# Kernel tuning notes

Hardware: AMD Instinct MI355X
Metric: run time of the kernel (lower is better)

## Reference

```python
import jax, jax.numpy as jnp
import numpy as np

D = 128      # memory_dim
L = 64       # segment_len
SCALE = 1.0 / np.sqrt(D)
LN_EPS = 1e-5


def _layernorm(x, g, b):
    mu = x.mean(-1, keepdims=True)
    var = ((x - mu) ** 2).mean(-1, keepdims=True)
    return (x - mu) * jax.lax.rsqrt(var + LN_EPS) * g + b


def setup_inputs() -> dict:
    key = jax.random.key(0)
    ks = jax.random.split(key, 8)
    B, T, Hd = 4, 4096, 2048
    w = 0.02  # init scale for weight matrices
    return {
        "H": jax.random.normal(ks[0], (B, T, Hd), jnp.float32),
        "M": jax.random.normal(ks[1], (B, D, D), jnp.float32),  # [B,K=128,D=128]
        "ln_g": jnp.ones((Hd,), jnp.float32),
        "ln_b": jnp.zeros((Hd,), jnp.float32),
        "W_eta_w": jax.random.normal(ks[2], (Hd,), jnp.float32) * w,
        "W_eta_b": jnp.full((1,), -5.0, jnp.float32),
        "sum_q": jax.random.normal(ks[3], (D,), jnp.float32),
        "sp_w": jax.random.normal(ks[4], (Hd, D), jnp.float32) * w,
        "sp_b": jnp.zeros((D,), jnp.float32),
        "eta_ch": jnp.ones((D,), jnp.float32),
        "temp": jnp.ones((1,), jnp.float32),
        "W_qkv": jax.random.normal(ks[5], (Hd, 3 * D), jnp.float32) * w,
    }


def reference(H, M, ln_g, ln_b, W_eta_w, W_eta_b, sum_q, sp_w, sp_b, eta_ch, temp, W_qkv):
    B, T, _ = H.shape
    K = M.shape[1]
    S = T // L  # T chosen divisible by segment_len (no-pad branch)

    Hn = _layernorm(H, ln_g, ln_b)                      # [B,T,Hd]

    # ---- write_memory ----
    H_mem = Hn @ sp_w + sp_b                            # [B,T,D]
    eta_tokens = jnp.einsum('bth,h->bt', Hn, W_eta_w) + W_eta_b  # [B,T]

    H_segs = H_mem.reshape(B, S, L, D)
    summary_scores = jnp.einsum('d,bsld->bsl', sum_q, H_segs) * SCALE
    summary_w = jax.nn.softmax(summary_scores, axis=-1)
    Z_seg = jnp.einsum('bsl,bsld->bsd', summary_w, H_segs)       # [B,S,D]

    eta_sig = jax.nn.sigmoid(eta_tokens)                          # [B,T]
    eta_seg = eta_sig.reshape(B, S, L).max(axis=-1)[..., None]    # [B,S,1]

    scores = jnp.einsum('bsd,bkd->bsk', Z_seg, M) * SCALE * jnp.exp(temp)
    A = jax.nn.softmax(scores, axis=-1)                           # [B,S,K]
    DeltaM = jnp.einsum('bsk,bsd->bkd', A, Z_seg * eta_seg)       # [B,K,D]

    eta_avg = eta_seg.mean(axis=1, keepdims=True)                 # [B,1,1]
    gate = eta_avg * jax.nn.sigmoid(eta_ch)                       # [B,1,D]
    M_new = (1.0 - gate) * M + DeltaM / S

    norm_sq = jnp.sum(DeltaM ** 2) / S
    # diversity loss on M_new
    Mn = M_new / jnp.maximum(jnp.linalg.norm(M_new, axis=-1, keepdims=True), 1e-12)
    sim = jnp.einsum('bkd,bjd->bkj', Mn, Mn) * (1.0 - jnp.eye(K, dtype=M.dtype))
    div_loss = jnp.mean(sim ** 2)
    loss = norm_sq * 0.01 + div_loss * 0.1

    # ---- read_memory (from updated memory; K<=1024 -> dense softmax path) ----
    Q_r = Hn @ W_qkv[:, 2 * D:]                                   # [B,T,D]
    r_scores = jnp.einsum('btd,bkd->btk', Q_r, M_new)
    A_r = jax.nn.softmax(r_scores * 2.0, axis=-1)
    C = jnp.einsum('btk,bkd->btd', A_r, M_new)                    # [B,T,D]

    return C, loss
```

## Files before the change

### kernel.cpp

```cpp
#include <hip/hip_runtime.h>
#include <hip/hip_bf16.h>
#include <math.h>

#define HD   2048
#define DD   128
#define TT   4096
#define BB   4
#define MT   (BB*TT)
#define LSEG 64
#define SSEG 64
#define NCOL 256
#define SCALE_D 0.088388347648318447f

typedef _Float16 half8 __attribute__((ext_vector_type(8)));
typedef _Float16 half4v __attribute__((ext_vector_type(4)));
typedef float    f32x4 __attribute__((ext_vector_type(4)));

__device__ __forceinline__ float sigmf(float x){ return 1.f/(1.f+__expf(-x)); }

__device__ __forceinline__ void glds16(const void* g, void* l) {
  __builtin_amdgcn_global_load_lds(
      (const __attribute__((address_space(1))) unsigned int*)g,
      (__attribute__((address_space(3))) unsigned int*)l, 16, 0, 0);
}

__global__ void k_pre(const float* __restrict__ ln_g, const float* __restrict__ ln_b,
                      const float* __restrict__ sp_w, const float* __restrict__ sp_b,
                      const float* __restrict__ W_qkv, const float* __restrict__ W_eta_w,
                      const float* __restrict__ W_eta_b,
                      _Float16* __restrict__ Bp, float* __restrict__ s_vec,
                      float* __restrict__ cb_vec, float* __restrict__ we2,
                      float* __restrict__ scal)
{
  __shared__ float red1[256], red2[256];
  int n = blockIdx.x, t = threadIdx.x;
  float sp = 0.f, cp = 0.f;
  if (n < NCOL) {
    for (int h = t; h < HD; h += 256) {
      float w = (n < DD) ? sp_w[(size_t)h*DD + n] : W_qkv[(size_t)h*384 + 256 + (n-DD)];
      float g = ln_g[h], b = ln_b[h];
      Bp[(size_t)n*HD + h] = (_Float16)(g*w);
      sp += g*w; cp += b*w;
    }
  } else {
    for (int h = t; h < HD; h += 256) {
      float w = W_eta_w[h];
      float g = ln_g[h], b = ln_b[h];
      we2[h] = g*w;
      sp += g*w; cp += b*w;
    }
  }
  red1[t] = sp; red2[t] = cp;
  __syncthreads();
  for (int o = 128; o > 0; o >>= 1) {
    if (t < o) { red1[t] += red1[t+o]; red2[t] += red2[t+o]; }
    __syncthreads();
  }
  if (t == 0) {
    if (n < NCOL) {
      s_vec[n]  = red1[0];
      cb_vec[n] = red2[0] + ((n < DD) ? sp_b[n] : 0.f);
    } else {
      scal[0] = red1[0];
      scal[1] = red2[0] + W_eta_b[0];
      scal[2] = 0.f; scal[3] = 0.f;
    }
  }
}

__launch_bounds__(512, 2)
__global__ void k01(const float* __restrict__ H, const _Float16* __restrict__ Bp,
                    const float* __restrict__ s_vec, const float* __restrict__ cb_vec,
                    const float* __restrict__ we2, const float* __restrict__ scal,
                    const float* __restrict__ sum_q, const float* __restrict__ Mmat,
                    const float* __restrict__ temp,
                    float* __restrict__ Q_r, float* __restrict__ Zeta,
                    float* __restrict__ A_seg, float* __restrict__ eta_seg)
{
  __shared__ __align__(16) char pool[81920];
  __shared__ float we_s[HD];
  __shared__ float smu[64], srs[64], seta[64];
  __shared__ float sq_s[128], w64_s[64], Zs[128], red_s[4];
  __shared__ float eta_sh_s;
  _Float16* sA  = (_Float16*)pool;
  _Float16* sB  = (_Float16*)(pool + 16384);
  float*    sHm = (float*)pool;

  int tid = threadIdx.x;
  int seg = blockIdx.x;
  int b   = seg >> 6;
  int m0  = seg * 64;
  int w = tid >> 6, lane = tid & 63;
  int wr = w >> 2, wc = w & 3;
  int fcol = lane & 15, kq = lane >> 4;

  for (int i = tid; i < HD/4; i += 512)
    ((float4*)we_s)[i] = ((const float4*)we2)[i];
  if (tid < 128) sq_s[tid] = sum_q[tid];
  float scal0 = scal[0], scal1 = scal[1];
  __syncthreads();

  int r_l = tid >> 3, s8 = tid & 7;
  const float* aptr = H + (size_t)(m0 + r_l)*HD + s8*8;
  int bn[4], bsl[4];
#pragma unroll
  for (int i = 0; i < 4; ++i) {
    int idx = i*512 + tid;
    bn[i]  = idx >> 3;
    bsl[i] = (idx & 7) ^ (bn[i] & 7);
  }

  f32x4 acc[2][4];
#pragma unroll
  for (int i = 0; i < 2; ++i)
#pragma unroll
    for (int j = 0; j < 4; ++j) acc[i][j] = (f32x4){0.f,0.f,0.f,0.f};
  float s1 = 0.f, s2 = 0.f, se = 0.f;

  float4 pa0 = *(const float4*)(aptr + 0);
  float4 pa1 = *(const float4*)(aptr + 4);
#pragma unroll
  for (int i = 0; i < 4; ++i)
    glds16(Bp + (size_t)bn[i]*HD + bsl[i]*8, sB + (size_t)(i*512 + tid)*8);

  for (int kt = 0; kt < 32; ++kt) {
    int cur = kt & 1;
    int k0 = kt*64;
    _Float16* sAc = sA + cur*4096;
    _Float16* sBc = sB + cur*16384;
    {
      float v[8] = {pa0.x,pa0.y,pa0.z,pa0.w, pa1.x,pa1.y,pa1.z,pa1.w};
      const float4* wv4 = (const float4*)(we_s + k0 + s8*8);
      float4 u0 = wv4[0], u1 = wv4[1];
      float uu[8] = {u0.x,u0.y,u0.z,u0.w, u1.x,u1.y,u1.z,u1.w};
      half8 h0;
#pragma unroll
      for (int j = 0; j < 8; ++j) {
        s1 += v[j]; s2 += v[j]*v[j]; se += v[j]*uu[j];
        h0[j] = (_Float16)v[j];
      }
      *(half8*)&sAc[r_l*64 + (s8 ^ (r_l & 7))*8] = h0;
    }
    if (kt < 31) {
      const float* ap = aptr + (kt+1)*64;
      pa0 = *(const float4*)(ap + 0);
      pa1 = *(const float4*)(ap + 4);
      asm volatile("s_waitcnt vmcnt(2) lgkmcnt(0)" ::: "memory");
    } else {
      asm volatile("s_waitcnt vmcnt(0) lgkmcnt(0)" ::: "memory");
    }
    __builtin_amdgcn_s_barrier();
    __builtin_amdgcn_sched_barrier(0);
    if (kt < 31) {
      _Float16* sBn = sB + (cur^1)*16384;
      const _Float16* bsrc = Bp + (k0 + 64);
#pragma unroll
      for (int i = 0; i < 4; ++i)
        glds16(bsrc + (size_t)bn[i]*HD + bsl[i]*8, sBn + (size_t)(i*512 + tid)*8);
    }
#pragma unroll
    for (int ks = 0; ks < 2; ++ks) {
      half8 af[2], bf[4];
#pragma unroll
      for (int rt = 0; rt < 2; ++rt) {
        int r = wr*32 + rt*16 + fcol;
        int ch = (ks*4 + kq) ^ (r & 7);
        af[rt] = *(half8*)&sAc[r*64 + ch*8];
      }
#pragma unroll
      for (int ct = 0; ct < 4; ++ct) {
        int n = wc*64 + ct*16 + fcol;
        int ch = (ks*4 + kq) ^ (n & 7);
        bf[ct] = *(half8*)&sBc[n*64 + ch*8];
      }
#pragma unroll
      for (int rt = 0; rt < 2; ++rt)
#pragma unroll
        for (int ct = 0; ct < 4; ++ct)
          acc[rt][ct] = __builtin_amdgcn_mfma_f32_16x16x32_f16(af[rt], bf[ct], acc[rt][ct], 0,0,0);
    }
  }

  s1 += __shfl_xor(s1, 1); s1 += __shfl_xor(s1, 2); s1 += __shfl_xor(s1, 4);
  s2 += __shfl_xor(s2, 1); s2 += __shfl_xor(s2, 2); s2 += __shfl_xor(s2, 4);
  se += __shfl_xor(se, 1); se += __shfl_xor(se, 2); se += __shfl_xor(se, 4);
  if (s8 == 0) {
    float mu   = s1 * (1.f/HD);
    float var  = s2 * (1.f/HD) - mu*mu;
    float rstd = rsqrtf(var + 1e-5f);
    smu[r_l] = mu; srs[r_l] = rstd;
    seta[r_l] = rstd*(se - mu*scal0) + scal1;
  }
  __syncthreads();

#pragma unroll
  for (int ct = 0; ct < 4; ++ct) {
    int nl = wc*64 + ct*16 + fcol;
    float sn = s_vec[nl], cbn = cb_vec[nl];
#pragma unroll
    for (int rt = 0; rt < 2; ++rt)
#pragma unroll
      for (int r = 0; r < 4; ++r) {
        int m = wr*32 + rt*16 + kq*4 + r;
        sHm[m*260 + nl] = srs[m]*(acc[rt][ct][r] - smu[m]*sn) + cbn;
      }
  }
  __syncthreads();

#pragma unroll
  for (int j = 0; j < 4; ++j) {
    int idx = j*512 + tid;
    int row = idx >> 5, c4 = (idx & 31)*4;
    *(float4*)&Q_r[(size_t)(m0 + row)*DD + c4] = *(float4*)&sHm[row*260 + 128 + c4];
  }

  if (w == 0) {
    float sc = 0.f;
    const float4* hrow = (const float4*)&sHm[lane*260];
#pragma unroll
    for (int d4 = 0; d4 < 32; ++d4) {
      float4 hv = hrow[d4];
      float4 qv = *(const float4*)&sq_s[d4*4];
      sc += hv.x*qv.x + hv.y*qv.y + hv.z*qv.z + hv.w*qv.w;
    }
    sc *= SCALE_D;
    float mx = sc;
    for (int o = 32; o > 0; o >>= 1) mx = fmaxf(mx, __shfl_xor(mx, o));
    float e = __expf(sc - mx);
    float sm = e;
    for (int o = 32; o > 0; o >>= 1) sm += __shfl_xor(sm, o);
    w64_s[lane] = e / sm;
  } else if (w == 1) {
    float ev = seta[lane];
    for (int o = 32; o > 0; o >>= 1) ev = fmaxf(ev, __shfl_xor(ev, o));
    if (lane == 0) { float es = sigmf(ev); eta_sh_s = es; eta_seg[seg] = es; }
  }
  __syncthreads();

  if (tid < 128) {
    float z = 0.f;
    for (int l = 0; l < 64; ++l) z += w64_s[l]*sHm[l*260 + tid];
    Zs[tid] = z;
    Zeta[(size_t)seg*DD + tid] = z * eta_sh_s;
  }
  __syncthreads();

  float sc2 = 0.f;
  if (tid < 128) {
    const float4* mrow = (const float4*)(Mmat + ((size_t)b*DD + tid)*DD);
#pragma unroll
    for (int d4 = 0; d4 < 32; ++d4) {
      float4 mv = mrow[d4];
      sc2 += mv.x*Zs[d4*4] + mv.y*Zs[d4*4+1] + mv.z*Zs[d4*4+2] + mv.w*Zs[d4*4+3];
    }
    sc2 *= SCALE_D * __expf(temp[0]);
    float mx = sc2;
    for (int o = 32; o > 0; o >>= 1) mx = fmaxf(mx, __shfl_xor(mx, o));
    if (lane == 0) red_s[w] = mx;
  }
  __syncthreads();
  float ev2 = 0.f;
  if (tid < 128) {
    float mx = fmaxf(red_s[0], red_s[1]);
    ev2 = __expf(sc2 - mx);
    float sm = ev2;
    for (int o = 32; o > 0; o >>= 1) sm += __shfl_xor(sm, o);
    if (lane == 0) red_s[2 + w] = sm;
  }
  __syncthreads();
  if (tid < 128) {
    float smt = red_s[2] + red_s[3];
    A_seg[(size_t)seg*DD + tid] = ev2 / smt;
  }
}

__global__ void k2b(const float* __restrict__ A_seg, const float* __restrict__ Zeta,
                    const float* __restrict__ eta_seg, const float* __restrict__ Mmat,
                    const float* __restrict__ eta_ch,
                    float* __restrict__ M_new, float* __restrict__ rns_arr,
                    float* __restrict__ scal)
{
  __shared__ float As[64][33];
  __shared__ __align__(16) float Zsl[64*128];
  __shared__ float rowp[32][8];
  __shared__ float eta_av;
  __shared__ float redb[4];
  int tid = threadIdx.x;
  int b = blockIdx.x >> 2, kq = blockIdx.x & 3;
  for (int i = tid; i < 64*32; i += 256) {
    int s = i >> 5, j = i & 31;
    As[s][j] = A_seg[((size_t)b*SSEG + s)*DD + kq*32 + j];
  }
  const float4* z4 = (const float4*)(Zeta + (size_t)b*SSEG*DD);
  float4* zs4 = (float4*)Zsl;
  for (int i = tid; i < 64*32; i += 256) zs4[i] = z4[i];
  if (tid < 64) {
    float ev = eta_seg[(size_t)b*SSEG + tid];
    for (int o=32;o>0;o>>=1) ev += __shfl_xor(ev, o);
    if (tid == 0) eta_av = ev * (1.f/SSEG);
  }
  __syncthreads();
  int kl = tid & 31, dg = tid >> 5;
  int k = kq*32 + kl, d0 = dg*16;
  float dm[16];
#pragma unroll
  for (int j=0;j<16;j++) dm[j]=0.f;
  for (int s = 0; s < 64; ++s) {
    float a = As[s][kl];
    const float* zr = &Zsl[s*128 + d0];
#pragma unroll
    for (int j=0;j<16;j++) dm[j] += a * zr[j];
  }
  float nsq = 0.f;
#pragma unroll
  for (int j=0;j<16;j++) nsq += dm[j]*dm[j];
  float eav = eta_av;
  float mn[16];
  float ss = 0.f;
#pragma unroll
  for (int j=0;j<16;j++) {
    int d = d0 + j;
    float gate = eav * sigmf(eta_ch[d]);
    float v = (1.f - gate)*Mmat[((size_t)b*DD + k)*DD + d] + dm[j]*(1.f/SSEG);
    mn[j] = v; ss += v*v;
  }
#pragma unroll
  for (int j=0;j<16;j+=4) {
    float4 v4; v4.x=mn[j]; v4.y=mn[j+1]; v4.z=mn[j+2]; v4.w=mn[j+3];
    *(float4*)&M_new[((size_t)b*DD + k)*DD + d0 + j] = v4;
  }
  rowp[kl][dg] = ss;
  for (int o=1;o<64;o<<=1) nsq += __shfl_xor(nsq, o);
  if ((tid&63)==0) redb[tid>>6] = nsq;
  __syncthreads();
  if (tid == 0) atomicAdd(&scal[2], redb[0]+redb[1]+redb[2]+redb[3]);
  if (tid < 32) {
    float t2 = 0.f;
#pragma unroll
    for (int g=0; g<8; ++g) t2 += rowp[tid][g];
    float nrm = sqrtf(t2);
    rns_arr[(size_t)b*DD + kq*32 + tid] = 1.f / fmaxf(nrm, 1e-12f);
  }
}

__global__ void k2d(const float* __restrict__ M_new, const float* __restrict__ rns_arr,
                    float* __restrict__ scal)
{
  __shared__ float kr[4][128];
  __shared__ float redb[4];
  int tid = threadIdx.x;
  int b = blockIdx.x >> 5, kq = blockIdx.x & 31;
  for (int i = tid; i < 4*128; i += 256) {
    int ki = i >> 7, d = i & 127;
    kr[ki][d] = M_new[((size_t)b*DD + kq*4 + ki)*DD + d];
  }
  __syncthreads();
  int j = tid & 127, kh = tid >> 7;
  const float* mj = &M_new[((size_t)b*DD + j)*DD];
  float rj = rns_arr[(size_t)b*DD + j];
  float dv = 0.f;
#pragma unroll
  for (int ki2 = 0; ki2 < 2; ++ki2) {
    int kil = kh*2 + ki2;
    int kk = kq*4 + kil;
    float dot = 0.f;
    for (int d = 0; d < 128; d += 4) {
      float4 a = *(const float4*)(mj + d);
      dot += a.x*kr[kil][d] + a.y*kr[kil][d+1] + a.z*kr[kil][d+2] + a.w*kr[kil][d+3];
    }
    if (kk != j) {
      float sv = dot * rj * rns_arr[(size_t)b*DD + kk];
      dv += sv*sv;
    }
  }
  for (int o=1;o<64;o<<=1) dv += __shfl_xor(dv, o);
  if ((tid&63)==0) redb[tid>>6] = dv;
  __syncthreads();
  if (tid==0) atomicAdd(&scal[3], redb[0]+redb[1]+redb[2]+redb[3]);
}

__launch_bounds__(256, 1)
__global__ void k3(const float* __restrict__ Q_r, const float* __restrict__ M_new,
                   const float* __restrict__ scal, float* __restrict__ out)
{
  __shared__ __align__(16) _Float16 Mq[128*132];
  __shared__ __align__(16) _Float16 Mt[128*136];
  __shared__ __align__(16) _Float16 Ps[64*132];
  int tid = threadIdx.x;
  int b = blockIdx.x >> 6, tile = blockIdx.x & 63;
  int t0 = tile*64;
  if (blockIdx.x == 0 && tid == 0) {
    float loss = 0.01f*(scal[2]*(1.f/SSEG)) + 0.1f*(scal[3]*(1.f/(BB*DD*DD)));
    out[(size_t)MT*DD] = loss;
  }
  const float4* m4 = (const float4*)(M_new + (size_t)b*DD*DD);
#pragma unroll
  for (int it = 0; it < 4; ++it) {
    int sb = it*256 + tid;
    int rb = sb & 31, cb = sb >> 5;
    int r0 = rb*4, c0 = cb*4;
    float a[4][4];
#pragma unroll
    for (int j = 0; j < 4; ++j) {
      float4 v = m4[(size_t)(r0+j)*32 + cb];
      a[j][0]=v.x; a[j][1]=v.y; a[j][2]=v.z; a[j][3]=v.w;
    }
#pragma unroll
    for (int j = 0; j < 4; ++j) {
      half4v h; h.x=(_Float16)a[j][0]; h.y=(_Float16)a[j][1];
                h.z=(_Float16)a[j][2]; h.w=(_Float16)a[j][3];
      *(half4v*)&Mq[(r0+j)*132 + c0] = h;
    }
#pragma unroll
    for (int j2 = 0; j2 < 4; ++j2) {
      half4v h; h.x=(_Float16)a[0][j2]; h.y=(_Float16)a[1][j2];
                h.z=(_Float16)a[2][j2]; h.w=(_Float16)a[3][j2];
      *(half4v*)&Mt[(c0+j2)*136 + r0] = h;
    }
  }
  int w = tid >> 6, lane = tid & 63;
  int fcol = lane & 15, kq = lane >> 4;
  int tokA = t0 + w*16 + fcol;
  size_t qbase = ((size_t)b*TT + tokA)*DD;
  half8 af[4];
#pragma unroll
  for (int ks = 0; ks < 4; ++ks) {
    float4 q0 = *(const float4*)&Q_r[qbase + ks*32 + kq*8];
    float4 q1 = *(const float4*)&Q_r[qbase + ks*32 + kq*8 + 4];
    half8 h;
    h[0]=(_Float16)q0.x; h[1]=(_Float16)q0.y; h[2]=(_Float16)q0.z; h[3]=(_Float16)q0.w;
    h[4]=(_Float16)q1.x; h[5]=(_Float16)q1.y; h[6]=(_Float16)q1.z; h[7]=(_Float16)q1.w;
    af[ks] = h;
  }
  __syncthreads();
  f32x4 sacc[8];
#pragma unroll
  for (int nt = 0; nt < 8; ++nt) sacc[nt] = (f32x4){0.f,0.f,0.f,0.f};
#pragma unroll
  for (int nt = 0; nt < 8; ++nt)
#pragma unroll
    for (int ks = 0; ks < 4; ++ks) {
      half8 bf = *(half8*)&Mq[(nt*16 + fcol)*132 + ks*32 + kq*8];
      sacc[nt] = __builtin_amdgcn_mfma_f32_16x16x32_f16(af[ks], bf, sacc[nt], 0,0,0);
    }
#pragma unroll
  for (int nt = 0; nt < 8; ++nt)
#pragma unroll
    for (int r = 0; r < 4; ++r) sacc[nt][r] *= 2.f;
  float mx[4], sm[4];
#pragma unroll
  for (int r = 0; r < 4; ++r) {
    float m = sacc[0][r];
#pragma unroll
    for (int nt = 1; nt < 8; ++nt) m = fmaxf(m, sacc[nt][r]);
#pragma unroll
    for (int o = 1; o < 16; o <<= 1) m = fmaxf(m, __shfl_xor(m, o));
    mx[r] = m;
  }
#pragma unroll
  for (int r = 0; r < 4; ++r) sm[r] = 0.f;
#pragma unroll
  for (int nt = 0; nt < 8; ++nt)
#pragma unroll
    for (int r = 0; r < 4; ++r) {
      float e = __expf(sacc[nt][r] - mx[r]);
      sacc[nt][r] = e; sm[r] += e;
    }
#pragma unroll
  for (int r = 0; r < 4; ++r) {
    float s = sm[r];
#pragma unroll
    for (int o = 1; o < 16; o <<= 1) s += __shfl_xor(s, o);
    sm[r] = 1.f / s;
  }
#pragma unroll
  for (int nt = 0; nt < 8; ++nt)
#pragma unroll
    for (int r = 0; r < 4; ++r) {
      int tk = w*16 + kq*4 + r;
      Ps[tk*132 + nt*16 + fcol] = (_Float16)(sacc[nt][r]*sm[r]);
    }
  __syncthreads();
  half8 pf[4];
#pragma unroll
  for (int ks = 0; ks < 4; ++ks)
    pf[ks] = *(half8*)&Ps[(w*16 + fcol)*132 + ks*32 + kq*8];
  f32x4 cacc[8];
#pragma unroll
  for (int nt = 0; nt < 8; ++nt) cacc[nt] = (f32x4){0.f,0.f,0.f,0.f};
#pragma unroll
  for (int nt = 0; nt < 8; ++nt)
#pragma unroll
    for (int ks = 0; ks < 4; ++ks) {
      half8 bf = *(half8*)&Mt[(nt*16 + fcol)*136 + ks*32 + kq*8];
      cacc[nt] = __builtin_amdgcn_mfma_f32_16x16x32_f16(pf[ks], bf, cacc[nt], 0,0,0);
    }
#pragma unroll
  for (int nt = 0; nt < 8; ++nt)
#pragma unroll
    for (int r = 0; r < 4; ++r) {
      int tk = t0 + w*16 + kq*4 + r;
      out[((size_t)b*TT + tk)*DD + nt*16 + fcol] = cacc[nt][r];
    }
}

extern "C" void kernel_launch(void* const* d_in, const int* in_sizes, int n_in,
                              void* d_out, int out_size, void* d_ws, size_t ws_size,
                              hipStream_t stream)
{
  (void)in_sizes; (void)n_in; (void)out_size; (void)ws_size;
  const float* H       = (const float*)d_in[0];
  const float* Mmat    = (const float*)d_in[1];
  const float* ln_g    = (const float*)d_in[2];
  const float* ln_b    = (const float*)d_in[3];
  const float* W_eta_w = (const float*)d_in[4];
  const float* W_eta_b = (const float*)d_in[5];
  const float* sum_q   = (const float*)d_in[6];
  const float* sp_w    = (const float*)d_in[7];
  const float* sp_b    = (const float*)d_in[8];
  const float* eta_ch  = (const float*)d_in[9];
  const float* temp    = (const float*)d_in[10];
  const float* W_qkv   = (const float*)d_in[11];
  float* out           = (float*)d_out;

  char* wsb = (char*)d_ws;
  size_t off = 0;
  auto alloc = [&](size_t bytes) -> void* {
    void* p = wsb + off;
    off = (off + bytes + 255) & ~(size_t)255;
    return p;
  };
  _Float16* Bp   = (_Float16*)alloc((size_t)NCOL*HD*2);
  float* s_vec   = (float*)alloc(NCOL*4);
  float* cb_vec  = (float*)alloc(NCOL*4);
  float* we2     = (float*)alloc(HD*4);
  float* scal    = (float*)alloc(4*4);
  float* Q_r     = (float*)alloc((size_t)MT*DD*4);
  float* Zeta    = (float*)alloc((size_t)BB*SSEG*DD*4);
  float* A_seg   = (float*)alloc((size_t)BB*SSEG*DD*4);
  float* eta_seg = (float*)alloc((size_t)BB*SSEG*4);
  float* M_new   = (float*)alloc((size_t)BB*DD*DD*4);
  float* rns_arr = (float*)alloc((size_t)BB*DD*4);

  hipLaunchKernelGGL(k_pre, dim3(NCOL+1), dim3(256), 0, stream,
                     ln_g, ln_b, sp_w, sp_b, W_qkv, W_eta_w, W_eta_b,
                     Bp, s_vec, cb_vec, we2, scal);
  hipLaunchKernelGGL(k01, dim3(MT/64), dim3(512), 0, stream,
                     H, Bp, s_vec, cb_vec, we2, scal, sum_q, Mmat, temp,
                     Q_r, Zeta, A_seg, eta_seg);
  hipLaunchKernelGGL(k2b, dim3(16), dim3(256), 0, stream,
                     A_seg, Zeta, eta_seg, Mmat, eta_ch, M_new, rns_arr, scal);
  hipLaunchKernelGGL(k2d, dim3(128), dim3(256), 0, stream,
                     M_new, rns_arr, scal);
  hipLaunchKernelGGL(k3, dim3(256), dim3(256), 0, stream,
                     Q_r, M_new, scal, out);
}
```

Before: 96.36 us.

## Triple-buffer B tiles and prefetch H two steps ahead in fused GEMM

```diff
diff --git a/kernel.cpp b/kernel.cpp
--- a/kernel.cpp
+++ b/kernel.cpp
@@ -77,7 +77,7 @@
                     float* __restrict__ Q_r, float* __restrict__ Zeta,
                     float* __restrict__ A_seg, float* __restrict__ eta_seg)
 {
-  __shared__ __align__(16) char pool[81920];
+  __shared__ __align__(16) char pool[114688];
   __shared__ float we_s[HD];
   __shared__ float smu[64], srs[64], seta[64];
   __shared__ float sq_s[128], w64_s[64], Zs[128], red_s[4];
@@ -117,69 +117,90 @@
     for (int j = 0; j < 4; ++j) acc[i][j] = (f32x4){0.f,0.f,0.f,0.f};
   float s1 = 0.f, s2 = 0.f, se = 0.f;
 
-  float4 pa0 = *(const float4*)(aptr + 0);
-  float4 pa1 = *(const float4*)(aptr + 4);
+  float4 paE0 = *(const float4*)(aptr + 0);
+  float4 paE1 = *(const float4*)(aptr + 4);
 #pragma unroll
   for (int i = 0; i < 4; ++i)
     glds16(Bp + (size_t)bn[i]*HD + bsl[i]*8, sB + (size_t)(i*512 + tid)*8);
-
-  for (int kt = 0; kt < 32; ++kt) {
-    int cur = kt & 1;
-    int k0 = kt*64;
-    _Float16* sAc = sA + cur*4096;
-    _Float16* sBc = sB + cur*16384;
-    {
-      float v[8] = {pa0.x,pa0.y,pa0.z,pa0.w, pa1.x,pa1.y,pa1.z,pa1.w};
-      const float4* wv4 = (const float4*)(we_s + k0 + s8*8);
-      float4 u0 = wv4[0], u1 = wv4[1];
-      float uu[8] = {u0.x,u0.y,u0.z,u0.w, u1.x,u1.y,u1.z,u1.w};
-      half8 h0;
-#pragma unroll
-      for (int j = 0; j < 8; ++j) {
-        s1 += v[j]; s2 += v[j]*v[j]; se += v[j]*uu[j];
-        h0[j] = (_Float16)v[j];
-      }
-      *(half8*)&sAc[r_l*64 + (s8 ^ (r_l & 7))*8] = h0;
-    }
-    if (kt < 31) {
-      const float* ap = aptr + (kt+1)*64;
-      pa0 = *(const float4*)(ap + 0);
-      pa1 = *(const float4*)(ap + 4);
-      asm volatile("s_waitcnt vmcnt(2) lgkmcnt(0)" ::: "memory");
-    } else {
-      asm volatile("s_waitcnt vmcnt(0) lgkmcnt(0)" ::: "memory");
-    }
-    __builtin_amdgcn_s_barrier();
-    __builtin_amdgcn_sched_barrier(0);
-    if (kt < 31) {
-      _Float16* sBn = sB + (cur^1)*16384;
-      const _Float16* bsrc = Bp + (k0 + 64);
-#pragma unroll
-      for (int i = 0; i < 4; ++i)
-        glds16(bsrc + (size_t)bn[i]*HD + bsl[i]*8, sBn + (size_t)(i*512 + tid)*8);
-    }
-#pragma unroll
-    for (int ks = 0; ks < 2; ++ks) {
-      half8 af[2], bf[4];
-#pragma unroll
-      for (int rt = 0; rt < 2; ++rt) {
-        int r = wr*32 + rt*16 + fcol;
-        int ch = (ks*4 + kq) ^ (r & 7);
-        af[rt] = *(half8*)&sAc[r*64 + ch*8];
-      }
-#pragma unroll
-      for (int ct = 0; ct < 4; ++ct) {
-        int n = wc*64 + ct*16 + fcol;
-        int ch = (ks*4 + kq) ^ (n & 7);
-        bf[ct] = *(half8*)&sBc[n*64 + ch*8];
-      }
-#pragma unroll
-      for (int rt = 0; rt < 2; ++rt)
-#pragma unroll
-        for (int ct = 0; ct < 4; ++ct)
-          acc[rt][ct] = __builtin_amdgcn_mfma_f32_16x16x32_f16(af[rt], bf[ct], acc[rt][ct], 0,0,0);
-    }
-  }
+  float4 paO0 = *(const float4*)(aptr + 64);
+  float4 paO1 = *(const float4*)(aptr + 68);
+#pragma unroll
+  for (int i = 0; i < 4; ++i)
+    glds16(Bp + (size_t)bn[i]*HD + 64 + bsl[i]*8,
+           sB + 16384 + (size_t)(i*512 + tid)*8);
+
+  int cur3 = 0;
+
+#define KSTEP(KT, P0, P1, VMASM, PREFETCH, BISSUE)                            \
+  {                                                                           \
+    _Float16* sAc = sA + ((KT)&1)*4096;                                       \
+    _Float16* sBc = sB + cur3*16384;                                          \
+    int k0 = (KT)*64;                                                         \
+    float v[8] = {P0.x,P0.y,P0.z,P0.w, P1.x,P1.y,P1.z,P1.w};                  \
+    if (PREFETCH) {                                                           \
+      const float* ap_ = aptr + ((KT)+2)*64;                                  \
+      P0 = *(const float4*)(ap_ + 0);                                         \
+      P1 = *(const float4*)(ap_ + 4);                                         \
+    }                                                                         \
+    {                                                                         \
+      const float4* wv4 = (const float4*)(we_s + k0 + s8*8);                  \
+      float4 u0 = wv4[0], u1 = wv4[1];                                        \
+      float uu[8] = {u0.x,u0.y,u0.z,u0.w, u1.x,u1.y,u1.z,u1.w};               \
+      half8 h0;                                                               \
+      _Pragma("unroll")                                                       \
+      for (int j = 0; j < 8; ++j) {                                           \
+        s1 += v[j]; s2 += v[j]*v[j]; se += v[j]*uu[j];                        \
+        h0[j] = (_Float16)v[j];                                               \
+      }                                                                       \
+      *(half8*)&sAc[r_l*64 + (s8 ^ (r_l & 7))*8] = h0;                        \
+    }                                                                         \
+    asm volatile(VMASM ::: "memory");                                         \
+    __builtin_amdgcn_s_barrier();                                             \
+    __builtin_amdgcn_sched_barrier(0);                                        \
+    if (BISSUE) {                                                             \
+      int wb3 = cur3 + 2; if (wb3 >= 3) wb3 -= 3;                             \
+      _Float16* sBn = sB + wb3*16384;                                         \
+      const _Float16* bsrc = Bp + (k0 + 128);                                 \
+      _Pragma("unroll")                                                       \
+      for (int i = 0; i < 4; ++i)                                             \
+        glds16(bsrc + (size_t)bn[i]*HD + bsl[i]*8,                            \
+               sBn + (size_t)(i*512 + tid)*8);                                \
+      __builtin_amdgcn_sched_barrier(0);                                      \
+    }                                                                         \
+    __builtin_amdgcn_s_setprio(1);                                            \
+    _Pragma("unroll")                                                         \
+    for (int ks = 0; ks < 2; ++ks) {                                          \
+      half8 af[2], bf[4];                                                     \
+      _Pragma("unroll")                                                       \
+      for (int rt = 0; rt < 2; ++rt) {                                        \
+        int r = wr*32 + rt*16 + fcol;                                         \
+        int ch = (ks*4 + kq) ^ (r & 7);                                       \
+        af[rt] = *(half8*)&sAc[r*64 + ch*8];                                  \
+      }                                                                       \
+      _Pragma("unroll")                                                       \
+      for (int ct = 0; ct < 4; ++ct) {                                        \
+        int n = wc*64 + ct*16 + fcol;                                         \
+        int ch = (ks*4 + kq) ^ (n & 7);                                       \
+        bf[ct] = *(half8*)&sBc[n*64 + ch*8];                                  \
+      }                                                                       \
+      _Pragma("unroll")                                                       \
+      for (int rt = 0; rt < 2; ++rt)                                          \
+        _Pragma("unroll")                                                     \
+        for (int ct = 0; ct < 4; ++ct)                                        \
+          acc[rt][ct] = __builtin_amdgcn_mfma_f32_16x16x32_f16(af[rt], bf[ct], acc[rt][ct], 0,0,0); \
+    }                                                                         \
+    __builtin_amdgcn_s_setprio(0);                                            \
+    cur3 += 1; if (cur3 >= 3) cur3 -= 3;                                      \
+  }
+
+#pragma unroll 1
+  for (int kp = 0; kp < 15; ++kp) {
+    KSTEP(2*kp,   paE0, paE1, "s_waitcnt vmcnt(8) lgkmcnt(0)", 1, 1)
+    KSTEP(2*kp+1, paO0, paO1, "s_waitcnt vmcnt(8) lgkmcnt(0)", 1, 1)
+  }
+  KSTEP(30, paE0, paE1, "s_waitcnt vmcnt(6) lgkmcnt(0)", 0, 0)
+  KSTEP(31, paO0, paO1, "s_waitcnt vmcnt(0) lgkmcnt(0)", 0, 0)
+#undef KSTEP
 
   s1 += __shfl_xor(s1, 1); s1 += __shfl_xor(s1, 2); s1 += __shfl_xor(s1, 4);
   s2 += __shfl_xor(s2, 1); s2 += __shfl_xor(s2, 2); s2 += __shfl_xor(s2, 4);
```

After: 87.06 us. 9.7% less time.
